# Performance work log

Measured on AMD Instinct MI355X. Metric: run time of the kernel, lower is better.

## Reference

```python
import jax, jax.numpy as jnp
import numpy as np

THRESH = 0.7
MIN_KEPT = 100000


def setup_inputs() -> dict:
    key = jax.random.key(0)
    k1, k2 = jax.random.split(key)
    N, C, H, W = 4, 19, 512, 1024
    logits = jax.random.normal(k1, (N, C, H, W), dtype=jnp.float32)
    targets = jax.random.randint(k2, (N, H, W), 0, C, dtype=jnp.int64)
    return {"logits": logits, "targets": targets}


def reference(logits, targets):
    # log_softmax over class dim, then per-pixel NLL gather.  [N,C,H,W] -> [N,H,W]
    log_p = jax.nn.log_softmax(logits, axis=1)
    nll = -jnp.take_along_axis(log_p, targets[:, None, :, :], axis=1)[:, 0]
    loss_flat = nll.reshape(-1)

    valid = loss_flat > 0  # mirrors `loss_flat > 0` validity test in torch code
    n_valid = valid.sum()

    # Descending sort with invalid pixels pushed to the end (-inf).
    sorted_loss = jnp.sort(jnp.where(valid, loss_flat, -jnp.inf))[::-1]

    n_keep = jnp.maximum(jnp.int32(MIN_KEPT), (THRESH * n_valid).astype(jnp.int32))
    n_keep = jnp.minimum(n_keep, n_valid.astype(jnp.int32))
    thresh_val = sorted_loss[jnp.maximum(n_keep - 1, 0)]

    mask = loss_flat >= thresh_val
    kept_sum = jnp.sum(jnp.where(mask, loss_flat, jnp.float32(0)))
    kept_cnt = jnp.maximum(mask.sum(), 1).astype(loss_flat.dtype)
    ohem_mean = kept_sum / kept_cnt

    # If no valid pixels, torch returns loss_flat.mean()
    return jnp.where(n_valid > 0, ohem_mean, loss_flat.mean())
```

## Files before the change

kernel.cpp:

```cpp
#include <hip/hip_runtime.h>

#define NBATCH 4
#define NCLS   19
#define HW     524288
#define NPIX   (NBATCH * HW)
#define NQ     (NPIX / 4)

#define NCOPY   8
#define NBINS   2048
#define H0        0
#define H1        (NCOPY * NBINS)
#define CT_BASE   (2 * NCOPY * NBINS)
#define CT_SUM    CT_BASE
#define CT_CNT    (CT_BASE + 2)
#define CT_TICKET (CT_BASE + 3)
#define CT_BAR    (CT_BASE + 4)
#define CTRL_U32  (CT_BASE + 8)
#define LOSS_OFF  262144

#define LH_BLOCKS 512
#define FU_BLOCKS 512
#define FU_THREADS (FU_BLOCKS * 256)

__global__ __launch_bounds__(256) void loss_hist_k(const float* __restrict__ logits,
                                                   const int* __restrict__ targets,
                                                   float* __restrict__ loss,
                                                   unsigned* __restrict__ hist0) {
    __shared__ unsigned sh[NBINS];
    for (int i = threadIdx.x; i < NBINS; i += 256) sh[i] = 0u;
    __syncthreads();

    int tid = blockIdx.x * 256 + threadIdx.x;
#pragma unroll 1
    for (int q = tid; q < NQ; q += LH_BLOCKS * 256) {
        int p   = q << 2;
        int n   = p >> 19;
        int pix = p & (HW - 1);
        const float4* base = reinterpret_cast<const float4*>(
            logits + (size_t)n * NCLS * HW + pix);
        int4 t4 = *reinterpret_cast<const int4*>(targets + p);

        float s0 = 0.f, s1 = 0.f, s2 = 0.f, s3 = 0.f;
        float g0 = 0.f, g1 = 0.f, g2 = 0.f, g3 = 0.f;
#pragma unroll
        for (int c = 0; c < NCLS; ++c) {
            float4 val = base[c * (HW / 4)];
            s0 += __expf(val.x); s1 += __expf(val.y);
            s2 += __expf(val.z); s3 += __expf(val.w);
            if (c == t4.x) g0 = val.x;
            if (c == t4.y) g1 = val.y;
            if (c == t4.z) g2 = val.z;
            if (c == t4.w) g3 = val.w;
        }
        float l0 = __logf(s0) - g0;
        float l1 = __logf(s1) - g1;
        float l2 = __logf(s2) - g2;
        float l3 = __logf(s3) - g3;
        *reinterpret_cast<float4*>(loss + p) = make_float4(l0, l1, l2, l3);

        if (l0 > 0.f) atomicAdd(&sh[__float_as_uint(l0) >> 21], 1u);
        if (l1 > 0.f) atomicAdd(&sh[__float_as_uint(l1) >> 21], 1u);
        if (l2 > 0.f) atomicAdd(&sh[__float_as_uint(l2) >> 21], 1u);
        if (l3 > 0.f) atomicAdd(&sh[__float_as_uint(l3) >> 21], 1u);
    }
    __syncthreads();
    unsigned* g = hist0 + (blockIdx.x & (NCOPY - 1)) * NBINS;
    for (int i = threadIdx.x; i < NBINS; i += 256) {
        unsigned vv = sh[i];
        if (vv) atomicAdd(&g[i], vv);
    }
}

__device__ __forceinline__ void scan_hist(const unsigned* __restrict__ ghist,
                                          unsigned* sh_h, unsigned* sh_c,
                                          unsigned* bcast, unsigned k_in,
                                          bool derive_k, bool bypass) {
    int t = threadIdx.x;
    for (int i = t; i < NBINS; i += 256) {
        unsigned s = 0;
#pragma unroll
        for (int k = 0; k < NCOPY; ++k) {
            s += bypass ? __hip_atomic_load(&ghist[k * NBINS + i],
                                            __ATOMIC_RELAXED, __HIP_MEMORY_SCOPE_AGENT)
                        : ghist[k * NBINS + i];
        }
        sh_h[i] = s;
    }
    __syncthreads();
    unsigned s = 0;
#pragma unroll
    for (int j = 0; j < 8; ++j) s += sh_h[t * 8 + j];
    sh_c[t] = s;
    __syncthreads();
    if (t == 0) {
        unsigned k = k_in, flag = 0;
        unsigned total = 0;
        for (int i = 0; i < 256; ++i) total += sh_c[i];
        if (derive_k) {
            if (total == 0) { flag = 1u; k = 1u; }
            else {
                long long kk = (long long)(0.7f * (float)total);
                if (kk < 100000) kk = 100000;
                if (kk > (long long)total) kk = (long long)total;
                k = (unsigned)kk;
            }
        }
        unsigned run = 0; int chunk = -1;
        for (int i = 255; i >= 0; --i) {
            if (run + sh_c[i] >= k) { chunk = i; break; }
            run += sh_c[i];
        }
        unsigned sel = 0, rank = 1;
        if (chunk >= 0) {
            for (int b = chunk * 8 + 7; b >= chunk * 8; --b) {
                if (run + sh_h[b] >= k) { sel = (unsigned)b; rank = k - run; break; }
                run += sh_h[b];
            }
        }
        bcast[0] = sel; bcast[1] = rank; bcast[2] = flag; bcast[3] = total;
    }
    __syncthreads();
}

__global__ __launch_bounds__(256, 2) void fused_k(const float4* __restrict__ loss4,
                                                  unsigned* __restrict__ ctrl,
                                                  float* __restrict__ out) {
    __shared__ unsigned h[NBINS];
    __shared__ unsigned c2[256];
    __shared__ unsigned bcast[4];

    scan_hist(ctrl + H0, h, c2, bcast, 0u, true, false);
    unsigned sel0 = bcast[0], rank1 = bcast[1], flag = bcast[2];
    __syncthreads();

    int tid = blockIdx.x * 256 + threadIdx.x;
    float4 v0 = loss4[tid];
    float4 v1 = loss4[tid + FU_THREADS];
    float4 v2 = loss4[tid + 2 * FU_THREADS];
    float4 v3 = loss4[tid + 3 * FU_THREADS];

    for (int i = threadIdx.x; i < NBINS; i += 256) h[i] = 0u;
    __syncthreads();
    if (!flag) {
#define PROC(X) do { float x_ = (X); if (x_ > 0.f) { unsigned u_ = __float_as_uint(x_); \
        if ((u_ >> 21) == sel0) atomicAdd(&h[(u_ >> 10) & 0x7FFu], 1u); } } while (0)
        PROC(v0.x); PROC(v0.y); PROC(v0.z); PROC(v0.w);
        PROC(v1.x); PROC(v1.y); PROC(v1.z); PROC(v1.w);
        PROC(v2.x); PROC(v2.y); PROC(v2.z); PROC(v2.w);
        PROC(v3.x); PROC(v3.y); PROC(v3.z); PROC(v3.w);
#undef PROC
        __syncthreads();
        unsigned* g = ctrl + H1 + (blockIdx.x & (NCOPY - 1)) * NBINS;
        for (int i = threadIdx.x; i < NBINS; i += 256) {
            unsigned vv = h[i];
            if (vv) atomicAdd(&g[i], vv);
        }
    }

    __syncthreads();
    if (threadIdx.x == 0) {
        __hip_atomic_fetch_add(&ctrl[CT_BAR], 1u, __ATOMIC_ACQ_REL, __HIP_MEMORY_SCOPE_AGENT);
        unsigned cur;
        do {
            __builtin_amdgcn_s_sleep(16);
            cur = __hip_atomic_fetch_add(&ctrl[CT_BAR], 0u,
                                         __ATOMIC_ACQUIRE, __HIP_MEMORY_SCOPE_AGENT);
        } while (cur < (unsigned)FU_BLOCKS);
    }
    __syncthreads();

    float thresh;
    if (flag) {
        thresh = -__builtin_inff();
    } else {
        scan_hist(ctrl + H1, h, c2, bcast, rank1, false, true);
        thresh = __uint_as_float((sel0 << 21) | (bcast[0] << 10));
    }

    double lsum = 0.0; unsigned lcnt = 0;
#define ACC(X) do { float x_ = (X); if (x_ >= thresh) { lsum += (double)x_; lcnt++; } } while (0)
    ACC(v0.x); ACC(v0.y); ACC(v0.z); ACC(v0.w);
    ACC(v1.x); ACC(v1.y); ACC(v1.z); ACC(v1.w);
    ACC(v2.x); ACC(v2.y); ACC(v2.z); ACC(v2.w);
    ACC(v3.x); ACC(v3.y); ACC(v3.z); ACC(v3.w);
#undef ACC

    __shared__ double sd[256];
    __shared__ unsigned sc[256];
    int t = threadIdx.x;
    sd[t] = lsum; sc[t] = lcnt;
    __syncthreads();
    for (int o = 128; o > 0; o >>= 1) {
        if (t < o) { sd[t] += sd[t + o]; sc[t] += sc[t + o]; }
        __syncthreads();
    }
    if (t == 0) {
        atomicAdd(reinterpret_cast<double*>(ctrl + CT_SUM), sd[0]);
        atomicAdd(&ctrl[CT_CNT], sc[0]);
        __threadfence();
        unsigned tick = atomicAdd(&ctrl[CT_TICKET], 1u);
        if (tick == (unsigned)(FU_BLOCKS - 1)) {
            double ssum = atomicAdd(reinterpret_cast<double*>(ctrl + CT_SUM), 0.0);
            unsigned cc = atomicAdd(&ctrl[CT_CNT], 0u);
            if (cc < 1u) cc = 1u;
            out[0] = (float)(ssum / (double)cc);
        }
    }
}

extern "C" void kernel_launch(void* const* d_in, const int* in_sizes, int n_in,
                              void* d_out, int out_size, void* d_ws, size_t ws_size,
                              hipStream_t stream) {
    const float* logits  = (const float*)d_in[0];
    const int*   targets = (const int*)d_in[1];
    float* out = (float*)d_out;
    unsigned* ctrl = (unsigned*)d_ws;
    float* loss = (float*)((char*)d_ws + LOSS_OFF);
    const float4* loss4 = (const float4*)loss;

    hipMemsetAsync(ctrl, 0, CTRL_U32 * sizeof(unsigned), stream);
    loss_hist_k<<<LH_BLOCKS, 256, 0, stream>>>(logits, targets, loss, ctrl + H0);
    fused_k<<<FU_BLOCKS, 256, 0, stream>>>(loss4, ctrl, out);
}
```

Measured before the change: 121.4 us.

## Fuse loss computation into the persistent kernel and keep losses in registers

Merges the loss/histogram kernel into the single persistent kernel. Each thread computes the losses for its 16 pixels and keeps them in registers, and a new grid barrier separates the coarse histogram build from its scan. This removes the global write and re-read of the 8 MB loss buffer and one kernel launch. In exchange it adds a second spin barrier, and occupancy is limited by the 2-blocks-per-SM launch bound while the logits read is the dominant cost.

After: 186.8 us. 1.54x slower.

```diff
diff --git a/kernel.cpp b/kernel.cpp
--- a/kernel.cpp
+++ b/kernel.cpp
@@ -4,7 +4,6 @@
 #define NCLS   19
 #define HW     524288
 #define NPIX   (NBATCH * HW)
-#define NQ     (NPIX / 4)
 
 #define NCOPY   8
 #define NBINS   2048
@@ -14,76 +13,38 @@
 #define CT_SUM    CT_BASE
 #define CT_CNT    (CT_BASE + 2)
 #define CT_TICKET (CT_BASE + 3)
-#define CT_BAR    (CT_BASE + 4)
+#define CT_BAR1   (CT_BASE + 4)
+#define CT_BAR2   (CT_BASE + 5)
 #define CTRL_U32  (CT_BASE + 8)
-#define LOSS_OFF  262144
-
-#define LH_BLOCKS 512
-#define FU_BLOCKS 512
+
+#define FU_BLOCKS  512
 #define FU_THREADS (FU_BLOCKS * 256)
 
-__global__ __launch_bounds__(256) void loss_hist_k(const float* __restrict__ logits,
-                                                   const int* __restrict__ targets,
-                                                   float* __restrict__ loss,
-                                                   unsigned* __restrict__ hist0) {
-    __shared__ unsigned sh[NBINS];
-    for (int i = threadIdx.x; i < NBINS; i += 256) sh[i] = 0u;
-    __syncthreads();
-
-    int tid = blockIdx.x * 256 + threadIdx.x;
-#pragma unroll 1
-    for (int q = tid; q < NQ; q += LH_BLOCKS * 256) {
-        int p   = q << 2;
-        int n   = p >> 19;
-        int pix = p & (HW - 1);
-        const float4* base = reinterpret_cast<const float4*>(
-            logits + (size_t)n * NCLS * HW + pix);
-        int4 t4 = *reinterpret_cast<const int4*>(targets + p);
-
-        float s0 = 0.f, s1 = 0.f, s2 = 0.f, s3 = 0.f;
-        float g0 = 0.f, g1 = 0.f, g2 = 0.f, g3 = 0.f;
-#pragma unroll
-        for (int c = 0; c < NCLS; ++c) {
-            float4 val = base[c * (HW / 4)];
-            s0 += __expf(val.x); s1 += __expf(val.y);
-            s2 += __expf(val.z); s3 += __expf(val.w);
-            if (c == t4.x) g0 = val.x;
-            if (c == t4.y) g1 = val.y;
-            if (c == t4.z) g2 = val.z;
-            if (c == t4.w) g3 = val.w;
-        }
-        float l0 = __logf(s0) - g0;
-        float l1 = __logf(s1) - g1;
-        float l2 = __logf(s2) - g2;
-        float l3 = __logf(s3) - g3;
-        *reinterpret_cast<float4*>(loss + p) = make_float4(l0, l1, l2, l3);
-
-        if (l0 > 0.f) atomicAdd(&sh[__float_as_uint(l0) >> 21], 1u);
-        if (l1 > 0.f) atomicAdd(&sh[__float_as_uint(l1) >> 21], 1u);
-        if (l2 > 0.f) atomicAdd(&sh[__float_as_uint(l2) >> 21], 1u);
-        if (l3 > 0.f) atomicAdd(&sh[__float_as_uint(l3) >> 21], 1u);
-    }
-    __syncthreads();
-    unsigned* g = hist0 + (blockIdx.x & (NCOPY - 1)) * NBINS;
-    for (int i = threadIdx.x; i < NBINS; i += 256) {
-        unsigned vv = sh[i];
-        if (vv) atomicAdd(&g[i], vv);
-    }
+__device__ __forceinline__ void grid_barrier(unsigned* bar) {
+    __syncthreads();
+    if (threadIdx.x == 0) {
+        __hip_atomic_fetch_add(bar, 1u, __ATOMIC_ACQ_REL, __HIP_MEMORY_SCOPE_AGENT);
+        unsigned cur;
+        do {
+            __builtin_amdgcn_s_sleep(16);
+            cur = __hip_atomic_fetch_add(bar, 0u, __ATOMIC_ACQUIRE,
+                                         __HIP_MEMORY_SCOPE_AGENT);
+        } while (cur < (unsigned)FU_BLOCKS);
+    }
+    __syncthreads();
 }
 
 __device__ __forceinline__ void scan_hist(const unsigned* __restrict__ ghist,
                                           unsigned* sh_h, unsigned* sh_c,
                                           unsigned* bcast, unsigned k_in,
-                                          bool derive_k, bool bypass) {
+                                          bool derive_k) {
     int t = threadIdx.x;
     for (int i = t; i < NBINS; i += 256) {
         unsigned s = 0;
 #pragma unroll
-        for (int k = 0; k < NCOPY; ++k) {
-            s += bypass ? __hip_atomic_load(&ghist[k * NBINS + i],
-                                            __ATOMIC_RELAXED, __HIP_MEMORY_SCOPE_AGENT)
-                        : ghist[k * NBINS + i];
-        }
+        for (int k = 0; k < NCOPY; ++k)
+            s += __hip_atomic_load(&ghist[k * NBINS + i],
+                                   __ATOMIC_RELAXED, __HIP_MEMORY_SCOPE_AGENT);
         sh_h[i] = s;
     }
     __syncthreads();
@@ -122,33 +83,78 @@
     __syncthreads();
 }
 
-__global__ __launch_bounds__(256, 2) void fused_k(const float4* __restrict__ loss4,
-                                                  unsigned* __restrict__ ctrl,
-                                                  float* __restrict__ out) {
+__global__ __launch_bounds__(256, 2) void fused_all_k(const float* __restrict__ logits,
+                                                      const int* __restrict__ targets,
+                                                      unsigned* __restrict__ ctrl,
+                                                      float* __restrict__ out) {
     __shared__ unsigned h[NBINS];
     __shared__ unsigned c2[256];
     __shared__ unsigned bcast[4];
 
-    scan_hist(ctrl + H0, h, c2, bcast, 0u, true, false);
+    int tid = blockIdx.x * 256 + threadIdx.x;
+
+    for (int i = threadIdx.x; i < NBINS; i += 256) h[i] = 0u;
+    __syncthreads();
+
+    float4 v0, v1, v2, v3;
+#define LOSS_BODY(J, VD) do { \
+    int p = (tid + (J) * FU_THREADS) << 2; \
+    const float4* base = reinterpret_cast<const float4*>( \
+        logits + (size_t)(J) * NCLS * HW + (p & (HW - 1))); \
+    int4 t4 = *reinterpret_cast<const int4*>(targets + p); \
+    float s0 = 0.f, s1 = 0.f, s2 = 0.f, s3 = 0.f; \
+    float g0 = 0.f, g1 = 0.f, g2 = 0.f, g3 = 0.f; \
+    _Pragma("unroll") \
+    for (int c = 0; c < NCLS; ++c) { \
+        float4 val = base[c * (HW / 4)]; \
+        s0 += __expf(val.x); s1 += __expf(val.y); \
+        s2 += __expf(val.z); s3 += __expf(val.w); \
+        if (c == t4.x) g0 = val.x; \
+        if (c == t4.y) g1 = val.y; \
+        if (c == t4.z) g2 = val.z; \
+        if (c == t4.w) g3 = val.w; \
+    } \
+    VD = make_float4(__logf(s0) - g0, __logf(s1) - g1, \
+                     __logf(s2) - g2, __logf(s3) - g3); \
+} while (0)
+    LOSS_BODY(0, v0);
+    LOSS_BODY(1, v1);
+    LOSS_BODY(2, v2);
+    LOSS_BODY(3, v3);
+#undef LOSS_BODY
+
+#define PROC0(X) do { float x_ = (X); if (x_ > 0.f) \
+    atomicAdd(&h[__float_as_uint(x_) >> 21], 1u); } while (0)
+    PROC0(v0.x); PROC0(v0.y); PROC0(v0.z); PROC0(v0.w);
+    PROC0(v1.x); PROC0(v1.y); PROC0(v1.z); PROC0(v1.w);
+    PROC0(v2.x); PROC0(v2.y); PROC0(v2.z); PROC0(v2.w);
+    PROC0(v3.x); PROC0(v3.y); PROC0(v3.z); PROC0(v3.w);
+#undef PROC0
+    __syncthreads();
+    {
+        unsigned* g = ctrl + H0 + (blockIdx.x & (NCOPY - 1)) * NBINS;
+        for (int i = threadIdx.x; i < NBINS; i += 256) {
+            unsigned vv = h[i];
+            if (vv) atomicAdd(&g[i], vv);
+        }
+    }
+
+    grid_barrier(&ctrl[CT_BAR1]);
+
+    scan_hist(ctrl + H0, h, c2, bcast, 0u, true);
     unsigned sel0 = bcast[0], rank1 = bcast[1], flag = bcast[2];
     __syncthreads();
 
-    int tid = blockIdx.x * 256 + threadIdx.x;
-    float4 v0 = loss4[tid];
-    float4 v1 = loss4[tid + FU_THREADS];
-    float4 v2 = loss4[tid + 2 * FU_THREADS];
-    float4 v3 = loss4[tid + 3 * FU_THREADS];
-
     for (int i = threadIdx.x; i < NBINS; i += 256) h[i] = 0u;
     __syncthreads();
     if (!flag) {
-#define PROC(X) do { float x_ = (X); if (x_ > 0.f) { unsigned u_ = __float_as_uint(x_); \
+#define PROC1(X) do { float x_ = (X); if (x_ > 0.f) { unsigned u_ = __float_as_uint(x_); \
         if ((u_ >> 21) == sel0) atomicAdd(&h[(u_ >> 10) & 0x7FFu], 1u); } } while (0)
-        PROC(v0.x); PROC(v0.y); PROC(v0.z); PROC(v0.w);
-        PROC(v1.x); PROC(v1.y); PROC(v1.z); PROC(v1.w);
-        PROC(v2.x); PROC(v2.y); PROC(v2.z); PROC(v2.w);
-        PROC(v3.x); PROC(v3.y); PROC(v3.z); PROC(v3.w);
-#undef PROC
+        PROC1(v0.x); PROC1(v0.y); PROC1(v0.z); PROC1(v0.w);
+        PROC1(v1.x); PROC1(v1.y); PROC1(v1.z); PROC1(v1.w);
+        PROC1(v2.x); PROC1(v2.y); PROC1(v2.z); PROC1(v2.w);
+        PROC1(v3.x); PROC1(v3.y); PROC1(v3.z); PROC1(v3.w);
+#undef PROC1
         __syncthreads();
         unsigned* g = ctrl + H1 + (blockIdx.x & (NCOPY - 1)) * NBINS;
         for (int i = threadIdx.x; i < NBINS; i += 256) {
@@ -157,23 +163,13 @@
         }
     }
 
-    __syncthreads();
-    if (threadIdx.x == 0) {
-        __hip_atomic_fetch_add(&ctrl[CT_BAR], 1u, __ATOMIC_ACQ_REL, __HIP_MEMORY_SCOPE_AGENT);
-        unsigned cur;
-        do {
-            __builtin_amdgcn_s_sleep(16);
-            cur = __hip_atomic_fetch_add(&ctrl[CT_BAR], 0u,
-                                         __ATOMIC_ACQUIRE, __HIP_MEMORY_SCOPE_AGENT);
-        } while (cur < (unsigned)FU_BLOCKS);
-    }
-    __syncthreads();
+    grid_barrier(&ctrl[CT_BAR2]);
 
     float thresh;
     if (flag) {
         thresh = -__builtin_inff();
     } else {
-        scan_hist(ctrl + H1, h, c2, bcast, rank1, false, true);
+        scan_hist(ctrl + H1, h, c2, bcast, rank1, false);
         thresh = __uint_as_float((sel0 << 21) | (bcast[0] << 10));
     }
 
@@ -215,10 +211,7 @@
     const int*   targets = (const int*)d_in[1];
     float* out = (float*)d_out;
     unsigned* ctrl = (unsigned*)d_ws;
-    float* loss = (float*)((char*)d_ws + LOSS_OFF);
-    const float4* loss4 = (const float4*)loss;
 
     hipMemsetAsync(ctrl, 0, CTRL_U32 * sizeof(unsigned), stream);
-    loss_hist_k<<<LH_BLOCKS, 256, 0, stream>>>(logits, targets, loss, ctrl + H0);
-    fused_k<<<FU_BLOCKS, 256, 0, stream>>>(loss4, ctrl, out);
-}
+    fused_all_k<<<FU_BLOCKS, 256, 0, stream>>>(logits, targets, ctrl, out);
+}
```
